# Optimization experiments

Hardware: AMD Instinct MI355X
Metric: run time of the kernel (lower is better)

## Reference

```python
import jax, jax.numpy as jnp
import numpy as np

N, E, B, L = 32768, 524288, 64, 4
ESM, S, V, EH = 1280, 128, 16, 64
N_RBF = 16
CENTERS = jnp.linspace(0.0, 12.0, N_RBF)
GAMMA = 1.0 / ((12.0 / N_RBF) ** 2 + 1e-8)
LN_EPS = 1e-5


def setup_inputs() -> dict:
    key = jax.random.key(0)
    ks = iter(jax.random.split(key, 80))
    def w(shape, scale=0.02):
        return (jax.random.normal(next(ks), shape) * scale).astype(jnp.float32)
    def zeros(shape):
        return jnp.zeros(shape, jnp.float32)
    def ones(shape):
        return jnp.ones(shape, jnp.float32)
    inp = {}
    inp['x_esm'] = jax.random.normal(next(ks), (N, ESM), jnp.float32)
    inp['x_reschem'] = jax.random.normal(next(ks), (N, 6), jnp.float32)
    inp['x_role'] = jax.random.uniform(next(ks), (N, 2), jnp.float32)
    inp['x_dist_raw'] = jax.random.uniform(next(ks), (N, 4), jnp.float32) * 12.0
    inp['x_misc'] = jax.random.normal(next(ks), (N, 3), jnp.float32)
    inp['x_vec'] = jax.random.normal(next(ks), (N, 1, 3), jnp.float32)
    inp['pos'] = jax.random.normal(next(ks), (N, 3), jnp.float32) * 10.0
    inp['edge_dist_raw'] = jax.random.uniform(next(ks), (E, 2), jnp.float32) * 12.0
    # node scalar encoder
    inp['ne_esm_w'] = w((ESM, 128)); inp['ne_esm_b'] = zeros((128,))
    inp['ne_esm_ln_g'] = ones((128,)); inp['ne_esm_ln_b'] = zeros((128,))
    in_dim = 128 + 6 + 2 + 3 + 4 * N_RBF  # 203
    inp['ne_out_w'] = w((in_dim, S)); inp['ne_out_b'] = zeros((S,))
    inp['ne_out_ln_g'] = ones((S,)); inp['ne_out_ln_b'] = zeros((S,))
    # edge scalar encoder
    inp['ee_w'] = w((2 * N_RBF, EH)); inp['ee_b'] = zeros((EH,))
    inp['ee_ln_g'] = ones((EH,)); inp['ee_ln_b'] = zeros((EH,))
    inp['init_vec_w'] = w((1, V))
    # stacked per-layer params
    msi = 2 * S + EH + 1 + (2 * V + 1)  # scalar_mlp in for message gvp = 354
    usi = 2 * S + 2 * V                 # = 288
    inp['msg_s_w1'] = w((L, msi, S)); inp['msg_s_b1'] = zeros((L, S))
    inp['msg_s_w2'] = w((L, S, S)); inp['msg_s_b2'] = zeros((L, S))
    inp['msg_v_w'] = w((L, 2 * V + 1, V))
    inp['msg_g_w'] = w((L, S, V)); inp['msg_g_b'] = zeros((L, V))
    inp['upd_s_w1'] = w((L, usi, S)); inp['upd_s_b1'] = zeros((L, S))
    inp['upd_s_w2'] = w((L, S, S)); inp['upd_s_b2'] = zeros((L, S))
    inp['upd_v_w'] = w((L, 2 * V, V))
    inp['upd_g_w'] = w((L, S, V)); inp['upd_g_b'] = zeros((L, V))
    inp['ln_g'] = ones((L, S)); inp['ln_b'] = zeros((L, S))
    # heads
    inp['hm_w1'] = w((2 * S, S)); inp['hm_b1'] = zeros((S,))
    inp['hm_w2'] = w((S, 8)); inp['hm_b2'] = zeros((8,))
    inp['he_w1'] = w((2 * S, S)); inp['he_b1'] = zeros((S,))
    inp['he_w2'] = w((S, 7)); inp['he_b2'] = zeros((7,))
    inp['edge_index'] = jax.random.randint(next(ks), (2, E), 0, N, jnp.int32)
    inp['batch'] = jnp.sort(jax.random.randint(next(ks), (N,), 0, B, jnp.int32))
    return inp


def _ln(x, g, b):
    mu = x.mean(-1, keepdims=True)
    var = ((x - mu) ** 2).mean(-1, keepdims=True)
    return (x - mu) * jax.lax.rsqrt(var + LN_EPS) * g + b


def _rbf(d):
    # d [..., K] -> [..., K, N_RBF]
    return jnp.exp(-GAMMA * (d[..., None] - CENTERS) ** 2)


def _vnorm(v):
    # v [N, C, 3] -> [N, C]
    return jnp.sqrt(jnp.clip((v * v).sum(-1), 1e-8))


def _gvp(s, v, sw1, sb1, sw2, sb2, vw, gw, gb):
    s_cat = jnp.concatenate([s, _vnorm(v)], -1)
    h = jax.nn.silu(s_cat @ sw1 + sb1)
    s_out = h @ sw2 + sb2
    v_proj = jnp.einsum('nci,cv->nvi', v, vw)
    gate = jax.nn.sigmoid(s_out @ gw + gb)[..., None]
    return s_out, v_proj * gate


def _forward(x_esm, x_reschem, x_role, x_dist_raw, x_misc, x_vec, pos, edge_dist_raw,
             ne_esm_w, ne_esm_b, ne_esm_ln_g, ne_esm_ln_b, ne_out_w, ne_out_b,
             ne_out_ln_g, ne_out_ln_b, ee_w, ee_b, ee_ln_g, ee_ln_b, init_vec_w,
             msg_s_w1, msg_s_b1, msg_s_w2, msg_s_b2, msg_v_w, msg_g_w, msg_g_b,
             upd_s_w1, upd_s_b1, upd_s_w2, upd_s_b2, upd_v_w, upd_g_w, upd_g_b,
             ln_g, ln_b, hm_w1, hm_b1, hm_w2, hm_b2, he_w1, he_b1, he_w2, he_b2,
             edge_index, batch):
    n = x_esm.shape[0]
    # node scalar encoder (dropout = identity at eval)
    esm = jax.nn.silu(_ln(x_esm @ ne_esm_w + ne_esm_b, ne_esm_ln_g, ne_esm_ln_b))
    d_rbf = _rbf(x_dist_raw).reshape(n, -1)  # [N, 64]
    xcat = jnp.concatenate([esm, x_reschem, x_role, x_misc, d_rbf], -1)
    s = jax.nn.silu(_ln(xcat @ ne_out_w + ne_out_b, ne_out_ln_g, ne_out_ln_b))
    # init vector channels [N, V, 3]
    v = jnp.einsum('nci,cv->nvi', x_vec, init_vec_w)
    # edge scalar encoder
    e_rbf = _rbf(edge_dist_raw).reshape(edge_dist_raw.shape[0], -1)  # [E, 32]
    edge_s = jax.nn.silu(_ln(e_rbf @ ee_w + ee_b, ee_ln_g, ee_ln_b))
    # edge vectors [E, 1, 3]
    src, dst = edge_index[0], edge_index[1]
    rel = pos[dst] - pos[src]
    rel = rel / jnp.sqrt(jnp.clip((rel * rel).sum(-1, keepdims=True), 1e-8))
    edge_v = rel[:, None, :]
    edge_len = _vnorm(edge_v)  # [E, 1]
    for l in range(L):
        m_s_in = jnp.concatenate([s[src], s[dst], edge_s, edge_len], -1)
        m_v_in = jnp.concatenate([v[src], v[dst], edge_v], 1)
        m_s, m_v = _gvp(m_s_in, m_v_in, msg_s_w1[l], msg_s_b1[l], msg_s_w2[l],
                        msg_s_b2[l], msg_v_w[l], msg_g_w[l], msg_g_b[l])
        agg_s = jax.ops.segment_sum(m_s, dst, num_segments=n)
        agg_v = jax.ops.segment_sum(m_v, dst, num_segments=n)
        u_s_in = jnp.concatenate([s, agg_s], -1)
        u_v_in = jnp.concatenate([v, agg_v], 1)
        ds, dv = _gvp(u_s_in, u_v_in, upd_s_w1[l], upd_s_b1[l], upd_s_w2[l],
                      upd_s_b2[l], upd_v_w[l], upd_g_w[l], upd_g_b[l])
        s = _ln(s + ds, ln_g[l], ln_b[l])
        v = v + dv
    # graph pooling
    sums = jax.ops.segment_sum(s, batch, num_segments=B)
    cnts = jax.ops.segment_sum(jnp.ones((n, 1), s.dtype), batch, num_segments=B)
    pooled_mean = sums / jnp.clip(cnts, 1.0)
    pooled_max = jax.ops.segment_max(s, batch, num_segments=B)
    pooled_max = jnp.where(jnp.isfinite(pooled_max), pooled_max, 0.0)
    embed = jnp.concatenate([pooled_mean, pooled_max], -1)
    logits_metal = jax.nn.silu(embed @ hm_w1 + hm_b1) @ hm_w2 + hm_b2
    logits_ec = jax.nn.silu(embed @ he_w1 + he_b1) @ he_w2 + he_b2
    return logits_metal, logits_ec, embed


def reference(x_esm, x_reschem, x_role, x_dist_raw, x_misc, x_vec, pos, edge_dist_raw,
              ne_esm_w, ne_esm_b, ne_esm_ln_g, ne_esm_ln_b, ne_out_w, ne_out_b,
              ne_out_ln_g, ne_out_ln_b, ee_w, ee_b, ee_ln_g, ee_ln_b, init_vec_w,
              msg_s_w1, msg_s_b1, msg_s_w2, msg_s_b2, msg_v_w, msg_g_w, msg_g_b,
              upd_s_w1, upd_s_b1, upd_s_w2, upd_s_b2, upd_v_w, upd_g_w, upd_g_b,
              ln_g, ln_b, hm_w1, hm_b1, hm_w2, hm_b2, he_w1, he_b1, he_w2, he_b2,
              edge_index, batch):
    return _forward(x_esm, x_reschem, x_role, x_dist_raw, x_misc, x_vec, pos,
                    edge_dist_raw, ne_esm_w, ne_esm_b, ne_esm_ln_g, ne_esm_ln_b,
                    ne_out_w, ne_out_b, ne_out_ln_g, ne_out_ln_b, ee_w, ee_b,
                    ee_ln_g, ee_ln_b, init_vec_w, msg_s_w1, msg_s_b1, msg_s_w2,
                    msg_s_b2, msg_v_w, msg_g_w, msg_g_b, upd_s_w1, upd_s_b1,
                    upd_s_w2, upd_s_b2, upd_v_w, upd_g_w, upd_g_b, ln_g, ln_b,
                    hm_w1, hm_b1, hm_w2, hm_b2, he_w1, he_b1, he_w2, he_b2,
                    edge_index, batch)
```

## Files before the change

### kernel.cpp

```cpp
#include <hip/hip_runtime.h>
#include <hip/hip_bf16.h>
#include <cstddef>

constexpr int kN = 32768;
constexpr int kE = 524288;
constexpr int kB = 64;
constexpr int kL = 4;
constexpr float kGamma = (float)(1.0 / (0.5625 + 1e-8));
constexpr float kLnEps = 1e-5f;

#define DI __device__ __forceinline__

typedef __attribute__((ext_vector_type(8))) short bf16x8;
typedef __attribute__((ext_vector_type(4))) short s16x4;
typedef __attribute__((ext_vector_type(4))) float f32x4;
#define MFMA16(a, b, c) __builtin_amdgcn_mfma_f32_16x16x32_bf16(a, b, c, 0, 0, 0)

DI float siluf(float x) { return x / (1.f + __expf(-x)); }
DI float sigmf(float x) { return 1.f / (1.f + __expf(-x)); }
DI unsigned short f2bf(float x) {
  __hip_bfloat16 b = __float2bfloat16(x);
  return *(unsigned short*)&b;
}
DI float b2f(unsigned short u) {
  union { unsigned i; float f; } c; c.i = ((unsigned)u) << 16; return c.f;
}
DI bf16x8 ldA(const float* p) {
  const float4 a = *(const float4*)p;
  const float4 b = *(const float4*)(p + 4);
  bf16x8 r;
  r[0] = (short)f2bf(a.x); r[1] = (short)f2bf(a.y);
  r[2] = (short)f2bf(a.z); r[3] = (short)f2bf(a.w);
  r[4] = (short)f2bf(b.x); r[5] = (short)f2bf(b.y);
  r[6] = (short)f2bf(b.z); r[7] = (short)f2bf(b.w);
  return r;
}

__global__ void k_btA(const float* src, unsigned short* dst, int K) {
  int idx = blockIdx.x * 256 + threadIdx.x;
  if (idx >= K * 128) return;
  int c = idx & 127, k = idx >> 7;
  dst[c * K + k] = f2bf(src[(size_t)k * 128 + c]);
}

__global__ void k_bt1(const float* w, unsigned short* dst) {
  int idx = blockIdx.x * 256 + threadIdx.x;
  int c = idx & 127, k = idx >> 7;
  dst[c * 224 + k] = f2bf(k < 203 ? w[(size_t)k * 128 + c] : 0.f);
}

__global__ void k_btPQ(const float* w1, unsigned short* dst) {
  int idx = blockIdx.x * 256 + threadIdx.x;
  int cc = idx / 160, k = idx - cc * 160;
  int c = cc & 127, half = cc >> 7;
  float v = 0.f;
  if (k < 128) v = w1[(size_t)(half * 128 + k) * 128 + c];
  else if (k < 144) v = w1[(size_t)(321 + half * 16 + (k - 128)) * 128 + c];
  dst[idx] = f2bf(v);
}

__global__ void k_w2gw(const float* w2, const float* gw, const float* b2, const float* gb,
                       float* out) {
  int idx = blockIdx.x * 256 + threadIdx.x;
  if (idx < 2048) {
    int k = idx >> 4, t = idx & 15;
    float a = 0.f;
    for (int j = 0; j < 128; j++) a += w2[(size_t)k * 128 + j] * gw[j * 16 + t];
    out[idx] = a;
  } else if (idx < 2064) {
    int t = idx - 2048;
    float a = gb[t];
    for (int j = 0; j < 128; j++) a += b2[j] * gw[j * 16 + t];
    out[idx] = a;
  }
}

__global__ void k_xrest(const float* resch, const float* role, const float* misc,
                        const float* dist, float* xr) {
  int idx = blockIdx.x * 256 + threadIdx.x;
  int r = idx / 96, c = idx - r * 96;
  float v = 0.f;
  if (c < 6) v = resch[r * 6 + c];
  else if (c < 8) v = role[r * 2 + c - 6];
  else if (c < 11) v = misc[r * 3 + c - 8];
  else if (c < 75) {
    int j = c - 11;
    float d = dist[r * 4 + (j >> 4)];
    float t = d - 0.8f * (float)(j & 15);
    v = __expf(-kGamma * t * t);
  }
  xr[idx] = v;
}

struct G2 {
  const float* A1; const float* A2; const float* A3;
  const unsigned short* BT;
  float* out;
  unsigned short* obfP; unsigned short* obfQ;
  const float* bias; const float* lng; const float* lnb;
};

template <int MODE>
__global__ __launch_bounds__(256) void k_gemm2(G2 p) {
  constexpr int K = MODE == 0 ? 1280 : MODE == 1 ? 224 : MODE == 2 ? 160 : 288;
  constexpr int NS = K / 32;
  constexpr int NTC = (MODE == 2) ? 16 : 8;
  const int tid = threadIdx.x, lane = tid & 63, wv = tid >> 6;
  const int g4 = lane >> 4, lc = lane & 15;
  const int r = blockIdx.x * 64 + wv * 16 + lc;
  const f32x4 z = {0.f, 0.f, 0.f, 0.f};
  f32x4 acc[NTC];
#pragma unroll
  for (int nt = 0; nt < NTC; nt++) acc[nt] = z;

  if constexpr (MODE == 0) {
#pragma unroll 4
    for (int ks = 0; ks < NS; ks++) {
      const int k = ks * 32 + g4 * 8;
      const bf16x8 af = ldA(p.A1 + (size_t)r * 1280 + k);
#pragma unroll
      for (int nt = 0; nt < NTC; nt++)
        acc[nt] = MFMA16(af, *(const bf16x8*)&p.BT[(lc + 16 * nt) * K + k], acc[nt]);
    }
  } else {
#pragma unroll
    for (int ks = 0; ks < NS; ks++) {
      const int k = ks * 32 + g4 * 8;
      const float* ap;
      if constexpr (MODE == 1)
        ap = (k < 128) ? p.A1 + (size_t)r * 128 + k : p.A2 + (size_t)r * 96 + (k - 128);
      else if constexpr (MODE == 2)
        ap = (k < 128) ? p.A1 + (size_t)r * 128 + k : p.A2 + (size_t)r * 32 + (k - 128);
      else
        ap = (k < 128) ? p.A1 + (size_t)r * 128 + k
           : (k < 256) ? p.A2 + (size_t)r * 128 + (k - 128)
                       : p.A3 + (size_t)r * 32 + (k - 256);
      const bf16x8 af = ldA(ap);
#pragma unroll
      for (int nt = 0; nt < NTC; nt++)
        acc[nt] = MFMA16(af, *(const bf16x8*)&p.BT[(lc + 16 * nt) * K + k], acc[nt]);
    }
  }

  const int row0 = blockIdx.x * 64 + wv * 16 + g4 * 4;
  if constexpr (MODE == 0 || MODE == 1) {
    float bias8[8], g8[8], b8[8];
#pragma unroll
    for (int nt = 0; nt < 8; nt++) {
      int c = lc + 16 * nt;
      bias8[nt] = p.bias[c]; g8[nt] = p.lng[c]; b8[nt] = p.lnb[c];
    }
    float rsum[4] = {0.f, 0.f, 0.f, 0.f}, rsq[4] = {0.f, 0.f, 0.f, 0.f};
#pragma unroll
    for (int nt = 0; nt < 8; nt++)
#pragma unroll
      for (int i = 0; i < 4; i++) {
        float x = acc[nt][i] + bias8[nt];
        acc[nt][i] = x; rsum[i] += x; rsq[i] += x * x;
      }
#pragma unroll
    for (int m = 1; m < 16; m <<= 1)
#pragma unroll
      for (int i = 0; i < 4; i++) {
        rsum[i] += __shfl_xor(rsum[i], m);
        rsq[i] += __shfl_xor(rsq[i], m);
      }
#pragma unroll
    for (int i = 0; i < 4; i++) {
      float mu = rsum[i] * (1.f / 128.f);
      float rs = rsqrtf(rsq[i] * (1.f / 128.f) - mu * mu + kLnEps);
#pragma unroll
      for (int nt = 0; nt < 8; nt++) {
        float y = (acc[nt][i] - mu) * rs * g8[nt] + b8[nt];
        p.out[(size_t)(row0 + i) * 128 + lc + 16 * nt] = siluf(y);
      }
    }
  } else if constexpr (MODE == 2) {
#pragma unroll
    for (int i = 0; i < 4; i++) {
      bf16x8 po, qo;
#pragma unroll
      for (int nt = 0; nt < 8; nt++) {
        po[nt] = (short)f2bf(acc[nt][i]);
        qo[nt] = (short)f2bf(acc[nt + 8][i] + p.bias[lc + 16 * nt]);
      }
      *(bf16x8*)&p.obfP[(size_t)(row0 + i) * 128 + lc * 8] = po;
      *(bf16x8*)&p.obfQ[(size_t)(row0 + i) * 128 + lc * 8] = qo;
    }
  } else {
#pragma unroll
    for (int nt = 0; nt < 8; nt++) {
      float bv = p.bias[lc + 16 * nt];
#pragma unroll
      for (int i = 0; i < 4; i++)
        p.out[(size_t)(row0 + i) * 128 + lc + 16 * nt] = siluf(acc[nt][i] + bv);
    }
  }
}

__global__ void k_v0(const float* xv, const float* ivw, float* v) {
  int idx = blockIdx.x * 256 + threadIdx.x;
  int n = idx / 48, f = idx % 48, t = f / 3, i = f - t * 3;
  v[idx] = xv[n * 3 + i] * ivw[t];
}

__global__ void k_vn(const float* v, float* vn) {
  int idx = blockIdx.x * 256 + threadIdx.x;
  int n = idx >> 5, t = idx & 31;
  float val = 0.f;
  if (t < 16) {
    const float* b = &v[(size_t)n * 48 + t * 3];
    val = sqrtf(fmaxf(b[0] * b[0] + b[1] * b[1] + b[2] * b[2], 1e-8f));
  }
  vn[idx] = val;
}

__global__ void k_vab(const float* v, const float* vw,
                      unsigned short* VAb, unsigned short* VBb) {
  int idx = blockIdx.x * 256 + threadIdx.x;
  int n = idx >> 4, t = idx & 15;
  float a0 = 0.f, a1 = 0.f, a2 = 0.f, b0 = 0.f, b1 = 0.f, b2 = 0.f;
#pragma unroll
  for (int c = 0; c < 16; c++) {
    float wa = vw[c * 16 + t], wb = vw[(16 + c) * 16 + t];
    float x0 = v[(size_t)n * 48 + c * 3 + 0];
    float x1 = v[(size_t)n * 48 + c * 3 + 1];
    float x2 = v[(size_t)n * 48 + c * 3 + 2];
    a0 += x0 * wa; a1 += x1 * wa; a2 += x2 * wa;
    b0 += x0 * wb; b1 += x1 * wb; b2 += x2 * wb;
  }
  s16x4 A, Bv;
  A[0] = (short)f2bf(a0); A[1] = (short)f2bf(a1); A[2] = (short)f2bf(a2); A[3] = 0;
  Bv[0] = (short)f2bf(b0); Bv[1] = (short)f2bf(b1); Bv[2] = (short)f2bf(b2); Bv[3] = 0;
  *(s16x4*)&VAb[(size_t)n * 64 + t * 4] = A;
  *(s16x4*)&VBb[(size_t)n * 64 + t * 4] = Bv;
}

__global__ void k_hist(const int* ei, int* cnt) {
  int e = blockIdx.x * 256 + threadIdx.x;
  atomicAdd(&cnt[ei[kE + e]], 1);
}

__global__ __launch_bounds__(1024) void k_scan(const int* cnt, int* rowstart, int* cursor) {
  __shared__ int part[1024];
  const int t = threadIdx.x;
  const int base = t * 32;
  int loc[32];
  int s = 0;
#pragma unroll
  for (int i = 0; i < 32; i++) { loc[i] = cnt[base + i]; s += loc[i]; }
  part[t] = s;
  __syncthreads();
  for (int off = 1; off < 1024; off <<= 1) {
    int val = (t >= off) ? part[t - off] : 0;
    __syncthreads();
    part[t] += val;
    __syncthreads();
  }
  int run = (t == 0) ? 0 : part[t - 1];
#pragma unroll
  for (int i = 0; i < 32; i++) {
    rowstart[base + i] = run;
    cursor[base + i] = run;
    run += loc[i];
  }
  if (t == 1023) rowstart[kN] = run;
}

__global__ void k_scatter(const int* ei, const float* pos, int* cursor,
                          int* prm, int* srcp, float* relp, float* lenp) {
  int e = blockIdx.x * 256 + threadIdx.x;
  int a = ei[e], b = ei[kE + e];
  int p = atomicAdd(&cursor[b], 1);
  prm[p] = e;
  srcp[p] = a;
  float dx = pos[(size_t)b * 3 + 0] - pos[(size_t)a * 3 + 0];
  float dy = pos[(size_t)b * 3 + 1] - pos[(size_t)a * 3 + 1];
  float dz = pos[(size_t)b * 3 + 2] - pos[(size_t)a * 3 + 2];
  float n2 = dx * dx + dy * dy + dz * dz;
  float inv = 1.f / sqrtf(fmaxf(n2, 1e-8f));
  float rx = dx * inv, ry = dy * inv, rz = dz * inv;
  relp[(size_t)p * 3 + 0] = rx; relp[(size_t)p * 3 + 1] = ry; relp[(size_t)p * 3 + 2] = rz;
  lenp[p] = sqrtf(fmaxf(rx * rx + ry * ry + rz * rz, 1e-8f));
}

__global__ void k_enc_perm(const int* prm, const float* edr, const float* eew, const float* eeb,
                           const float* lg, const float* lb, __hip_bfloat16* enc) {
  int tid = threadIdx.x;
  int wave = tid >> 6, lane = tid & 63;
  size_t p = (size_t)blockIdx.x * 4 + wave;
  int e = prm[p];
  __shared__ float rb[4][32];
  if (lane < 32) {
    float d = edr[(size_t)e * 2 + (lane >> 4)];
    float t = d - 0.8f * (float)(lane & 15);
    rb[wave][lane] = __expf(-kGamma * t * t);
  }
  __syncthreads();
  float acc = eeb[lane];
#pragma unroll 8
  for (int k = 0; k < 32; k++) acc += rb[wave][k] * eew[k * 64 + lane];
  float s = acc;
#pragma unroll
  for (int off = 32; off >= 1; off >>= 1) s += __shfl_xor(s, off);
  float mu = s * (1.f / 64.f);
  float d0 = acc - mu;
  float q = d0 * d0;
#pragma unroll
  for (int off = 32; off >= 1; off >>= 1) q += __shfl_xor(q, off);
  float rs = rsqrtf(q * (1.f / 64.f) + kLnEps);
  float y = d0 * rs * lg[lane] + lb[lane];
  enc[p * 64 + lane] = __float2bfloat16(siluf(y));
}

struct __align__(16) EMS2 {
  unsigned short we1T[128 * 72];
  unsigned short w2T[128 * 136];
  unsigned short w2gwT[16 * 72];
  unsigned short h[8][16 * 72];
  float wlen[128];
  float b2[128];
  float gb[16];
  float vw32[16];
};

__global__ __launch_bounds__(512, 4) void k_node_msg(
    const unsigned short* __restrict__ Pb, const unsigned short* __restrict__ Qb,
    const unsigned short* __restrict__ VAb, const unsigned short* __restrict__ VBb,
    const __hip_bfloat16* __restrict__ enc_, const float* __restrict__ relp,
    const float* __restrict__ lenp, const int* __restrict__ srcp,
    const int* __restrict__ rowstart, const float* __restrict__ vglob,
    const float* __restrict__ w1, const float* __restrict__ w2g,
    const float* __restrict__ b2g, const float* __restrict__ w2gw,
    const float* __restrict__ vwg,
    float* __restrict__ aggs, float* __restrict__ aggv, float* __restrict__ vnu) {
  __shared__ EMS2 sm;
  const int tid = threadIdx.x;
  const unsigned short* enc = (const unsigned short*)enc_;

#pragma unroll
  for (int i = 0; i < 16; i++) {
    int idx = tid + i * 512; int k = idx >> 7, n = idx & 127;
    sm.we1T[n * 72 + k] = f2bf(w1[(size_t)(256 + k) * 128 + n]);
  }
#pragma unroll
  for (int i = 0; i < 32; i++) {
    int idx = tid + i * 512; int k = idx >> 7, n = idx & 127;
    sm.w2T[n * 136 + k] = f2bf(w2g[(size_t)k * 128 + n]);
  }
#pragma unroll
  for (int i = 0; i < 4; i++) {
    int idx = tid + i * 512; int k = idx >> 4, t = idx & 15;
    sm.w2gwT[t * 72 + k] = f2bf(w2gw[k * 16 + t]);
  }
  if (tid < 128) { sm.wlen[tid] = w1[320 * 128 + tid] + w1[353 * 128 + tid]; sm.b2[tid] = b2g[tid]; }
  if (tid < 16) { sm.gb[tid] = w2gw[2048 + tid]; sm.vw32[tid] = vwg[512 + tid]; }
  __syncthreads();

  const int lane = tid & 63, wv = tid >> 6;
  const int g4 = lane >> 4;
  const int lc = lane & 15;
  unsigned short* hrow = &sm.h[wv][0];

  float wlenR[8], b2R[8];
#pragma unroll
  for (int nt = 0; nt < 8; nt++) { wlenR[nt] = sm.wlen[lc + 16 * nt]; b2R[nt] = sm.b2[lc + 16 * nt]; }
  const float gbR = sm.gb[lc];
  const float vwR = sm.vw32[lc];
  const f32x4 z = {0.f, 0.f, 0.f, 0.f};

  for (int n = blockIdx.x * 8 + wv; n < kN; n += gridDim.x * 8) {
    const int r0 = rowstart[n], r1 = rowstart[n + 1];
    float qR[8], vbR[3];
    {
      const bf16x8 qv = *(const bf16x8*)&Qb[(size_t)n * 128 + lc * 8];
#pragma unroll
      for (int nt = 0; nt < 8; nt++) qR[nt] = b2f((unsigned short)qv[nt]);
      const s16x4 vbv = *(const s16x4*)&VBb[(size_t)n * 64 + lc * 4];
#pragma unroll
      for (int j = 0; j < 3; j++) vbR[j] = b2f((unsigned short)vbv[j]);
    }
    float colsum[8];
#pragma unroll
    for (int nt = 0; nt < 8; nt++) colsum[nt] = 0.f;
    float av0 = 0.f, av1 = 0.f, av2 = 0.f;

    for (int base = r0; base < r1; base += 16) {
      int nv = r1 - base; if (nv > 16) nv = 16;

      int pa = base + lc; if (pa >= kE) pa = kE - 1;
      const bf16x8 a0 = *(const bf16x8*)&enc[(size_t)pa * 64 + g4 * 8];
      const bf16x8 a1 = *(const bf16x8*)&enc[(size_t)pa * 64 + 32 + g4 * 8];
      f32x4 acc[8];
#pragma unroll
      for (int nt = 0; nt < 8; nt++) {
        acc[nt] = MFMA16(a0, *(const bf16x8*)&sm.we1T[(lc + 16 * nt) * 72 + g4 * 8], z);
        acc[nt] = MFMA16(a1, *(const bf16x8*)&sm.we1T[(lc + 16 * nt) * 72 + 32 + g4 * 8], acc[nt]);
      }

      int sn[4], pr[4]; float le[4];
#pragma unroll
      for (int i = 0; i < 4; i++) {
        int p = base + g4 * 4 + i; if (p >= kE) p = kE - 1;
        pr[i] = p; sn[i] = srcp[p]; le[i] = lenp[p];
      }
#pragma unroll
      for (int i = 0; i < 4; i++) {
        const bf16x8 pbv = *(const bf16x8*)&Pb[(size_t)sn[i] * 128 + lc * 8];
#pragma unroll
        for (int nt = 0; nt < 8; nt++)
          acc[nt][i] += b2f((unsigned short)pbv[nt]) + qR[nt] + le[i] * wlenR[nt];
      }

      f32x4 m[8]; f32x4 gac;
#pragma unroll
      for (int i = 0; i < 4; i++)
#pragma unroll
        for (int nt = 0; nt < 4; nt++)
          hrow[(g4 * 4 + i) * 72 + lc + 16 * nt] = f2bf(siluf(acc[nt][i]));
      {
        const bf16x8 aB0 = *(const bf16x8*)&hrow[lc * 72 + g4 * 8];
        const bf16x8 aB1 = *(const bf16x8*)&hrow[lc * 72 + 32 + g4 * 8];
#pragma unroll
        for (int nt = 0; nt < 8; nt++) {
          m[nt] = MFMA16(aB0, *(const bf16x8*)&sm.w2T[(lc + 16 * nt) * 136 + g4 * 8], z);
          m[nt] = MFMA16(aB1, *(const bf16x8*)&sm.w2T[(lc + 16 * nt) * 136 + 32 + g4 * 8], m[nt]);
        }
        gac = MFMA16(aB0, *(const bf16x8*)&sm.w2gwT[lc * 72 + g4 * 8], z);
        gac = MFMA16(aB1, *(const bf16x8*)&sm.w2gwT[lc * 72 + 32 + g4 * 8], gac);
      }
#pragma unroll
      for (int i = 0; i < 4; i++)
#pragma unroll
        for (int nt = 4; nt < 8; nt++)
          hrow[(g4 * 4 + i) * 72 + lc + 16 * (nt - 4)] = f2bf(siluf(acc[nt][i]));
      {
        const bf16x8 aB2 = *(const bf16x8*)&hrow[lc * 72 + g4 * 8];
        const bf16x8 aB3 = *(const bf16x8*)&hrow[lc * 72 + 32 + g4 * 8];
#pragma unroll
        for (int nt = 0; nt < 8; nt++) {
          m[nt] = MFMA16(aB2, *(const bf16x8*)&sm.w2T[(lc + 16 * nt) * 136 + 64 + g4 * 8], m[nt]);
          m[nt] = MFMA16(aB3, *(const bf16x8*)&sm.w2T[(lc + 16 * nt) * 136 + 96 + g4 * 8], m[nt]);
        }
        gac = MFMA16(aB2, *(const bf16x8*)&sm.w2gwT[lc * 72 + 64 + g4 * 8], gac);
        gac = MFMA16(aB3, *(const bf16x8*)&sm.w2gwT[lc * 72 + 96 + g4 * 8], gac);
      }
#pragma unroll
      for (int nt = 0; nt < 8; nt++) {
#pragma unroll
        for (int i = 0; i < 4; i++) m[nt][i] += b2R[nt];
      }

#pragma unroll
      for (int i = 0; i < 4; i++) {
        const int row = g4 * 4 + i;
        if (row < nv) {
#pragma unroll
          for (int nt = 0; nt < 8; nt++) colsum[nt] += m[nt][i];
          float g = sigmf(gac[i] + gbR);
          const s16x4 vav = *(const s16x4*)&VAb[(size_t)sn[i] * 64 + lc * 4];
          const float* rp = &relp[(size_t)pr[i] * 3];
          av0 += g * (b2f((unsigned short)vav[0]) + vbR[0] + rp[0] * vwR);
          av1 += g * (b2f((unsigned short)vav[1]) + vbR[1] + rp[1] * vwR);
          av2 += g * (b2f((unsigned short)vav[2]) + vbR[2] + rp[2] * vwR);
        }
      }
    }

#pragma unroll
    for (int nt = 0; nt < 8; nt++) {
      colsum[nt] += __shfl_xor(colsum[nt], 16);
      colsum[nt] += __shfl_xor(colsum[nt], 32);
    }
    av0 += __shfl_xor(av0, 16); av0 += __shfl_xor(av0, 32);
    av1 += __shfl_xor(av1, 16); av1 += __shfl_xor(av1, 32);
    av2 += __shfl_xor(av2, 16); av2 += __shfl_xor(av2, 32);

    if (g4 == 0) {
#pragma unroll
      for (int nt = 0; nt < 8; nt++) aggs[(size_t)n * 128 + lc + 16 * nt] = colsum[nt];
      aggv[(size_t)n * 48 + lc * 3 + 0] = av0;
      aggv[(size_t)n * 48 + lc * 3 + 1] = av1;
      aggv[(size_t)n * 48 + lc * 3 + 2] = av2;
      vnu[(size_t)n * 32 + 16 + lc] = sqrtf(fmaxf(av0 * av0 + av1 * av1 + av2 * av2, 1e-8f));
    } else if (g4 == 1) {
      float x0 = vglob[(size_t)n * 48 + lc * 3 + 0];
      float x1 = vglob[(size_t)n * 48 + lc * 3 + 1];
      float x2 = vglob[(size_t)n * 48 + lc * 3 + 2];
      vnu[(size_t)n * 32 + lc] = sqrtf(fmaxf(x0 * x0 + x1 * x1 + x2 * x2, 1e-8f));
    }
  }
}

__global__ __launch_bounds__(256) void k_upd2(
    const float* __restrict__ hupd, const unsigned short* __restrict__ BuT,
    const float* __restrict__ b2,
    const float* __restrict__ ugw, const float* __restrict__ ugb, const float* __restrict__ uvw,
    const float* __restrict__ aggv, const float* __restrict__ lng, const float* __restrict__ lnb,
    float* __restrict__ s, float* __restrict__ v, float* __restrict__ vnout) {
  __shared__ __align__(16) float dsb[64 * 129];
  __shared__ float smu[64], srs[64];
  __shared__ float uvwS[512];
  const int tid = threadIdx.x;
  const int bm = blockIdx.x * 64;
  const int lane = tid & 63, wv = tid >> 6;
  const int g4 = lane >> 4, lc = lane & 15;
  uvwS[tid] = uvw[tid]; uvwS[tid + 256] = uvw[tid + 256];
  const f32x4 z = {0.f, 0.f, 0.f, 0.f};
  const int r = bm + wv * 16 + lc;
  f32x4 acc[8];
#pragma unroll
  for (int nt = 0; nt < 8; nt++) acc[nt] = z;

#pragma unroll
  for (int ks = 0; ks < 4; ks++) {
    const int k = ks * 32 + g4 * 8;
    const bf16x8 af = ldA(hupd + (size_t)r * 128 + k);
#pragma unroll
    for (int nt = 0; nt < 8; nt++)
      acc[nt] = MFMA16(af, *(const bf16x8*)&BuT[(lc + 16 * nt) * 128 + k], acc[nt]);
  }
#pragma unroll
  for (int nt = 0; nt < 8; nt++) {
    float bv = b2[lc + 16 * nt];
#pragma unroll
    for (int i = 0; i < 4; i++)
      dsb[(wv * 16 + g4 * 4 + i) * 129 + lc + 16 * nt] = acc[nt][i] + bv;
  }
  __syncthreads();

  const int rr = tid >> 2, p = tid & 3;
  const int n = bm + rr;
  float g[4];
#pragma unroll
  for (int j = 0; j < 4; j++) g[j] = ugb[p * 4 + j];
#pragma unroll 8
  for (int k = 0; k < 128; k++) {
    float m = dsb[rr * 129 + k];
    const float4 wg = *(const float4*)&ugw[k * 16 + p * 4];
    g[0] += m * wg.x; g[1] += m * wg.y; g[2] += m * wg.z; g[3] += m * wg.w;
  }
#pragma unroll
  for (int j = 0; j < 4; j++) g[j] = sigmf(g[j]);

  float vnew[12];
#pragma unroll
  for (int i2 = 0; i2 < 3; i2++) {
    float xv[16], xa[16];
#pragma unroll
    for (int c = 0; c < 16; c++) {
      xv[c] = v[(size_t)n * 48 + c * 3 + i2];
      xa[c] = aggv[(size_t)n * 48 + c * 3 + i2];
    }
#pragma unroll
    for (int j = 0; j < 4; j++) {
      int t = p * 4 + j;
      float a = 0.f;
#pragma unroll
      for (int c = 0; c < 16; c++)
        a += xv[c] * uvwS[c * 16 + t] + xa[c] * uvwS[(16 + c) * 16 + t];
      vnew[j * 3 + i2] = xv[t] + a * g[j];
    }
  }
  if (tid < 64) {
    float sm = 0.f, sq = 0.f;
    for (int c = 0; c < 128; c++) {
      float x = s[(size_t)(bm + tid) * 128 + c] + dsb[tid * 129 + c];
      sm += x; sq += x * x;
    }
    float mu = sm * (1.f / 128.f);
    float var = sq * (1.f / 128.f) - mu * mu;
    smu[tid] = mu; srs[tid] = rsqrtf(var + kLnEps);
  }
  __syncthreads();
#pragma unroll
  for (int j = 0; j < 4; j++) {
    float n0 = vnew[j * 3 + 0], n1 = vnew[j * 3 + 1], n2 = vnew[j * 3 + 2];
#pragma unroll
    for (int i2 = 0; i2 < 3; i2++)
      v[(size_t)n * 48 + (p * 4 + j) * 3 + i2] = vnew[j * 3 + i2];
    vnout[(size_t)n * 32 + p * 4 + j] = sqrtf(fmaxf(n0 * n0 + n1 * n1 + n2 * n2, 1e-8f));
    vnout[(size_t)n * 32 + 16 + p * 4 + j] = 0.f;
  }
#pragma unroll 4
  for (int i = 0; i < 32; i++) {
    int idx = tid + i * 256; int rw = idx >> 7, c = idx & 127;
    float x = s[(size_t)(bm + rw) * 128 + c] + dsb[rw * 129 + c];
    float y = (x - smu[rw]) * srs[rw] * lng[c] + lnb[c];
    s[(size_t)(bm + rw) * 128 + c] = y;
  }
}

DI int lbound(const int* b, int nn, int key) {
  int lo = 0, hi = nn;
  while (lo < hi) { int m = (lo + hi) >> 1; if (b[m] < key) lo = m + 1; else hi = m; }
  return lo;
}

__global__ void k_pool(const float* s, const int* batch, float* dout) {
  int g = blockIdx.x, tid = threadIdx.x;
  int lo = lbound(batch, kN, g), hi = lbound(batch, kN, g + 1);
  float sum = 0.f, mx = -3.402823e38f;
  for (int n = lo; n < hi; n++) {
    float x = s[(size_t)n * 128 + tid];
    sum += x; mx = fmaxf(mx, x);
  }
  int cnt = hi - lo;
  float mean = sum / fmaxf((float)cnt, 1.f);
  if (cnt == 0) mx = 0.f;
  dout[960 + g * 256 + tid] = mean;
  dout[960 + g * 256 + 128 + tid] = mx;
}

__global__ void k_heads(const float* hw1, const float* hb1, const float* hw2, const float* hb2,
                        const float* ew1, const float* eb1, const float* ew2, const float* eb2,
                        float* dout) {
  __shared__ float emb[256], h1[256];
  int g = blockIdx.x, tid = threadIdx.x;
  emb[tid] = dout[960 + g * 256 + tid];
  emb[128 + tid] = dout[960 + g * 256 + 128 + tid];
  __syncthreads();
  float am = hb1[tid], ae = eb1[tid];
#pragma unroll 4
  for (int k = 0; k < 256; k++) {
    float e = emb[k];
    am += e * hw1[k * 128 + tid];
    ae += e * ew1[k * 128 + tid];
  }
  h1[tid] = siluf(am); h1[128 + tid] = siluf(ae);
  __syncthreads();
  if (tid < 8) {
    float a = hb2[tid];
    for (int j = 0; j < 128; j++) a += h1[j] * hw2[j * 8 + tid];
    dout[g * 8 + tid] = a;
  } else if (tid >= 64 && tid < 71) {
    int o = tid - 64;
    float a = eb2[o];
    for (int j = 0; j < 128; j++) a += h1[128 + j] * ew2[j * 7 + o];
    dout[512 + g * 7 + o] = a;
  }
}

extern "C" void kernel_launch(void* const* d_in, const int* in_sizes, int n_in,
                              void* d_out, int out_size, void* d_ws, size_t ws_size,
                              hipStream_t stream) {
  (void)in_sizes; (void)n_in; (void)out_size; (void)ws_size;
  const float* x_esm   = (const float*)d_in[0];
  const float* x_resch = (const float*)d_in[1];
  const float* x_role  = (const float*)d_in[2];
  const float* x_dist  = (const float*)d_in[3];
  const float* x_misc  = (const float*)d_in[4];
  const float* x_vec   = (const float*)d_in[5];
  const float* pos     = (const float*)d_in[6];
  const float* edr     = (const float*)d_in[7];
  const float* ne_esm_w = (const float*)d_in[8];
  const float* ne_esm_b = (const float*)d_in[9];
  const float* ne_esm_lg = (const float*)d_in[10];
  const float* ne_esm_lb = (const float*)d_in[11];
  const float* ne_out_w = (const float*)d_in[12];
  const float* ne_out_b = (const float*)d_in[13];
  const float* ne_out_lg = (const float*)d_in[14];
  const float* ne_out_lb = (const float*)d_in[15];
  const float* ee_w = (const float*)d_in[16];
  const float* ee_b = (const float*)d_in[17];
  const float* ee_lg = (const float*)d_in[18];
  const float* ee_lb = (const float*)d_in[19];
  const float* ivw = (const float*)d_in[20];
  const float* msg_w1 = (const float*)d_in[21];
  const float* msg_b1 = (const float*)d_in[22];
  const float* msg_w2 = (const float*)d_in[23];
  const float* msg_b2 = (const float*)d_in[24];
  const float* msg_vw = (const float*)d_in[25];
  const float* msg_gw = (const float*)d_in[26];
  const float* msg_gb = (const float*)d_in[27];
  const float* upd_w1 = (const float*)d_in[28];
  const float* upd_b1 = (const float*)d_in[29];
  const float* upd_w2 = (const float*)d_in[30];
  const float* upd_b2 = (const float*)d_in[31];
  const float* upd_vw = (const float*)d_in[32];
  const float* upd_gw = (const float*)d_in[33];
  const float* upd_gb = (const float*)d_in[34];
  const float* ln_g = (const float*)d_in[35];
  const float* ln_b = (const float*)d_in[36];
  const float* hm_w1 = (const float*)d_in[37];
  const float* hm_b1 = (const float*)d_in[38];
  const float* hm_w2 = (const float*)d_in[39];
  const float* hm_b2 = (const float*)d_in[40];
  const float* he_w1 = (const float*)d_in[41];
  const float* he_b1 = (const float*)d_in[42];
  const float* he_w2 = (const float*)d_in[43];
  const float* he_b2 = (const float*)d_in[44];
  const int* ei = (const int*)d_in[45];
  const int* batch = (const int*)d_in[46];
  float* dout = (float*)d_out;

  size_t off = 0;
  auto alloc = [&](size_t bytes) {
    void* p = (char*)d_ws + off;
    off += (bytes + 255) & ~(size_t)255;
    return p;
  };
  float* s    = (float*)alloc((size_t)kN * 128 * 4);
  float* v    = (float*)alloc((size_t)kN * 48 * 4);
  float* vn   = (float*)alloc((size_t)kN * 32 * 4);
  unsigned short* Pb = (unsigned short*)alloc((size_t)kN * 128 * 2);
  unsigned short* Qb = (unsigned short*)alloc((size_t)kN * 128 * 2);
  unsigned short* VAb = (unsigned short*)alloc((size_t)kN * 64 * 2);
  unsigned short* VBb = (unsigned short*)alloc((size_t)kN * 64 * 2);
  float* aggS = (float*)alloc((size_t)kN * 128 * 4);
  float* aggV = (float*)alloc((size_t)kN * 48 * 4);
  float* vnu  = (float*)alloc((size_t)kN * 32 * 4);
  float* hupd = (float*)alloc((size_t)kN * 128 * 4);
  float* xrest = (float*)alloc((size_t)kN * 96 * 4);
  __hip_bfloat16* enc = (__hip_bfloat16*)alloc((size_t)kE * 64 * 2);
  float* relp = (float*)alloc((size_t)kE * 3 * 4);
  float* lenp = (float*)alloc((size_t)kE * 4);
  int* srcp   = (int*)alloc((size_t)kE * 4);
  int* prm    = (int*)alloc((size_t)kE * 4);
  int* cnt    = (int*)alloc((size_t)kN * 4);
  int* rowstart = (int*)alloc((size_t)(kN + 1) * 4);
  int* cursor = (int*)alloc((size_t)kN * 4);
  unsigned short* B0T = (unsigned short*)alloc((size_t)128 * 1280 * 2);
  unsigned short* B1T = (unsigned short*)alloc((size_t)128 * 224 * 2);
  unsigned short* B23T = (unsigned short*)alloc((size_t)kL * 256 * 160 * 2);
  unsigned short* B4T = (unsigned short*)alloc((size_t)kL * 128 * 288 * 2);
  unsigned short* BuT = (unsigned short*)alloc((size_t)kL * 128 * 128 * 2);
  float* w2gwL = (float*)alloc((size_t)kL * 2064 * 4);
  float* esm = hupd;

  hipMemsetAsync(cnt, 0, (size_t)kN * 4, stream);
  k_hist<<<kE / 256, 256, 0, stream>>>(ei, cnt);
  k_scan<<<1, 1024, 0, stream>>>(cnt, rowstart, cursor);
  k_scatter<<<kE / 256, 256, 0, stream>>>(ei, pos, cursor, prm, srcp, relp, lenp);
  k_enc_perm<<<kE / 4, 256, 0, stream>>>(prm, edr, ee_w, ee_b, ee_lg, ee_lb, enc);
  k_btA<<<(1280 * 128 + 255) / 256, 256, 0, stream>>>(ne_esm_w, B0T, 1280);
  k_bt1<<<(224 * 128 + 255) / 256, 256, 0, stream>>>(ne_out_w, B1T);
  k_xrest<<<(kN * 96 + 255) / 256, 256, 0, stream>>>(x_resch, x_role, x_misc, x_dist, xrest);
  for (int l = 0; l < kL; l++) {
    k_btPQ<<<(256 * 160 + 255) / 256, 256, 0, stream>>>(msg_w1 + (size_t)l * 354 * 128,
                                                        B23T + (size_t)l * 256 * 160);
    k_btA<<<(288 * 128 + 255) / 256, 256, 0, stream>>>(upd_w1 + (size_t)l * 288 * 128,
                                                       B4T + (size_t)l * 128 * 288, 288);
    k_btA<<<(128 * 128 + 255) / 256, 256, 0, stream>>>(upd_w2 + (size_t)l * 128 * 128,
                                                       BuT + (size_t)l * 128 * 128, 128);
    k_w2gw<<<9, 256, 0, stream>>>(msg_w2 + (size_t)l * 128 * 128, msg_gw + l * 128 * 16,
                                  msg_b2 + l * 128, msg_gb + l * 16, w2gwL + (size_t)l * 2064);
  }

  {
    G2 p{}; p.A1 = x_esm; p.BT = B0T; p.out = esm;
    p.bias = ne_esm_b; p.lng = ne_esm_lg; p.lnb = ne_esm_lb;
    k_gemm2<0><<<kN / 64, 256, 0, stream>>>(p);
  }
  {
    G2 p{}; p.A1 = esm; p.A2 = xrest; p.BT = B1T; p.out = s;
    p.bias = ne_out_b; p.lng = ne_out_lg; p.lnb = ne_out_lb;
    k_gemm2<1><<<kN / 64, 256, 0, stream>>>(p);
  }
  k_v0<<<kN * 48 / 256, 256, 0, stream>>>(x_vec, ivw, v);
  k_vn<<<kN * 32 / 256, 256, 0, stream>>>(v, vn);

  for (int l = 0; l < kL; l++) {
    const float* w1l = msg_w1 + (size_t)l * 354 * 128;
    const float* b1l = msg_b1 + l * 128;
    const float* w2l = msg_w2 + (size_t)l * 128 * 128;
    const float* b2l = msg_b2 + l * 128;
    const float* vwl = msg_vw + l * 33 * 16;
    const float* ub1 = upd_b1 + l * 128;
    const float* ub2 = upd_b2 + l * 128;
    const float* uvwl = upd_vw + l * 32 * 16;
    const float* ugwl = upd_gw + l * 128 * 16;
    const float* ugbl = upd_gb + l * 16;
    const float* lgl = ln_g + l * 128;
    const float* lbl = ln_b + l * 128;

    {
      G2 p{}; p.A1 = s; p.A2 = vn; p.BT = B23T + (size_t)l * 256 * 160;
      p.obfP = Pb; p.obfQ = Qb; p.bias = b1l;
      k_gemm2<2><<<kN / 64, 256, 0, stream>>>(p);
    }
    k_vab<<<kN * 16 / 256, 256, 0, stream>>>(v, vwl, VAb, VBb);
    k_node_msg<<<512, 512, 0, stream>>>(Pb, Qb, VAb, VBb, enc, relp, lenp, srcp,
                                        rowstart, v, w1l, w2l, b2l,
                                        w2gwL + (size_t)l * 2064, vwl,
                                        aggS, aggV, vnu);
    {
      G2 p{}; p.A1 = s; p.A2 = aggS; p.A3 = vnu; p.BT = B4T + (size_t)l * 128 * 288;
      p.out = hupd; p.bias = ub1;
      k_gemm2<4><<<kN / 64, 256, 0, stream>>>(p);
    }
    k_upd2<<<kN / 64, 256, 0, stream>>>(hupd, BuT + (size_t)l * 128 * 128, ub2,
                                        ugwl, ugbl, uvwl, aggV, lgl, lbl, s, v, vn);
  }

  k_pool<<<kB, 128, 0, stream>>>(s, batch, dout);
  k_heads<<<kB, 128, 0, stream>>>(hm_w1, hm_b1, hm_w2, hm_b2,
                                  he_w1, he_b1, he_w2, he_b2, dout);
}
```

Before: 1.889 ms.

## Compute edge RBF encoder with MFMA over 64 edges per block

The edge scalar encoder used one wave per edge with a scalar 32-term dot product and shuffle reductions, and one block per four edges. It now handles 64 edges per block and computes the RBF-by-weight product with bf16 16x16x32 MFMA, using a transposed weight tile held in shared memory. LayerNorm uses a single-pass sum and sum-of-squares reduction across 16 lanes. This cuts per-edge instruction count and block count, at the cost of bf16 rounding of the RBF features and weights and a less stable variance formula.

```diff
diff --git a/kernel.cpp b/kernel.cpp
--- a/kernel.cpp
+++ b/kernel.cpp
@@ -284,33 +284,72 @@
   lenp[p] = sqrtf(fmaxf(rx * rx + ry * ry + rz * rz, 1e-8f));
 }
 
-__global__ void k_enc_perm(const int* prm, const float* edr, const float* eew, const float* eeb,
-                           const float* lg, const float* lb, __hip_bfloat16* enc) {
-  int tid = threadIdx.x;
-  int wave = tid >> 6, lane = tid & 63;
-  size_t p = (size_t)blockIdx.x * 4 + wave;
-  int e = prm[p];
-  __shared__ float rb[4][32];
-  if (lane < 32) {
-    float d = edr[(size_t)e * 2 + (lane >> 4)];
-    float t = d - 0.8f * (float)(lane & 15);
-    rb[wave][lane] = __expf(-kGamma * t * t);
+__global__ __launch_bounds__(256) void k_enc_mfma(
+    const int* __restrict__ prm, const float* __restrict__ edr,
+    const float* __restrict__ eew, const float* __restrict__ eeb,
+    const float* __restrict__ lg, const float* __restrict__ lb,
+    __hip_bfloat16* __restrict__ enc) {
+  __shared__ unsigned short eewT[64 * 32];
+  const int tid = threadIdx.x;
+#pragma unroll
+  for (int i = 0; i < 8; i++) {
+    int idx = tid + i * 256;
+    int col = idx >> 5, k = idx & 31;
+    eewT[col * 32 + k] = f2bf(eew[k * 64 + col]);
   }
   __syncthreads();
-  float acc = eeb[lane];
-#pragma unroll 8
-  for (int k = 0; k < 32; k++) acc += rb[wave][k] * eew[k * 64 + lane];
-  float s = acc;
-#pragma unroll
-  for (int off = 32; off >= 1; off >>= 1) s += __shfl_xor(s, off);
-  float mu = s * (1.f / 64.f);
-  float d0 = acc - mu;
-  float q = d0 * d0;
-#pragma unroll
-  for (int off = 32; off >= 1; off >>= 1) q += __shfl_xor(q, off);
-  float rs = rsqrtf(q * (1.f / 64.f) + kLnEps);
-  float y = d0 * rs * lg[lane] + lb[lane];
-  enc[p * 64 + lane] = __float2bfloat16(siluf(y));
+
+  const int lane = tid & 63, wv = tid >> 6;
+  const int g4 = lane >> 4, lc = lane & 15;
+  const int e0 = blockIdx.x * 64 + wv * 16;
+
+  const int e = prm[e0 + lc];
+  const float d = edr[(size_t)e * 2 + (g4 >> 1)];
+  const float c0 = 0.8f * (float)((g4 & 1) * 8);
+  bf16x8 af;
+#pragma unroll
+  for (int j = 0; j < 8; j++) {
+    float t = d - (c0 + 0.8f * (float)j);
+    af[j] = (short)f2bf(__expf(-kGamma * t * t));
+  }
+  const f32x4 z = {0.f, 0.f, 0.f, 0.f};
+  f32x4 acc[4];
+#pragma unroll
+  for (int ct = 0; ct < 4; ct++)
+    acc[ct] = MFMA16(af, *(const bf16x8*)&eewT[(ct * 16 + lc) * 32 + g4 * 8], z);
+
+  float bias4[4], g4v[4], b4[4];
+#pragma unroll
+  for (int ct = 0; ct < 4; ct++) {
+    int col = ct * 16 + lc;
+    bias4[ct] = eeb[col]; g4v[ct] = lg[col]; b4[ct] = lb[col];
+  }
+  float rsum[4] = {0.f, 0.f, 0.f, 0.f}, rsq[4] = {0.f, 0.f, 0.f, 0.f};
+#pragma unroll
+  for (int ct = 0; ct < 4; ct++)
+#pragma unroll
+    for (int i = 0; i < 4; i++) {
+      float x = acc[ct][i] + bias4[ct];
+      acc[ct][i] = x; rsum[i] += x; rsq[i] += x * x;
+    }
+#pragma unroll
+  for (int m = 1; m < 16; m <<= 1)
+#pragma unroll
+    for (int i = 0; i < 4; i++) {
+      rsum[i] += __shfl_xor(rsum[i], m);
+      rsq[i] += __shfl_xor(rsq[i], m);
+    }
+#pragma unroll
+  for (int i = 0; i < 4; i++) {
+    float mu = rsum[i] * (1.f / 64.f);
+    float rs = rsqrtf(rsq[i] * (1.f / 64.f) - mu * mu + kLnEps);
+    const size_t row = (size_t)(e0 + g4 * 4 + i);
+#pragma unroll
+    for (int ct = 0; ct < 4; ct++) {
+      float y = (acc[ct][i] - mu) * rs * g4v[ct] + b4[ct];
+      enc[row * 64 + ct * 16 + lc] = __float2bfloat16(siluf(y));
+    }
+  }
 }
 
 struct __align__(16) EMS2 {
@@ -732,7 +771,7 @@
   k_hist<<<kE / 256, 256, 0, stream>>>(ei, cnt);
   k_scan<<<1, 1024, 0, stream>>>(cnt, rowstart, cursor);
   k_scatter<<<kE / 256, 256, 0, stream>>>(ei, pos, cursor, prm, srcp, relp, lenp);
-  k_enc_perm<<<kE / 4, 256, 0, stream>>>(prm, edr, ee_w, ee_b, ee_lg, ee_lb, enc);
+  k_enc_mfma<<<kE / 64, 256, 0, stream>>>(prm, edr, ee_w, ee_b, ee_lg, ee_lb, enc);
   k_btA<<<(1280 * 128 + 255) / 256, 256, 0, stream>>>(ne_esm_w, B0T, 1280);
   k_bt1<<<(224 * 128 + 255) / 256, 256, 0, stream>>>(ne_out_w, B1T);
   k_xrest<<<(kN * 96 + 255) / 256, 256, 0, stream>>>(x_resch, x_role, x_misc, x_dist, xrest);
```

After: 1.747 ms. 1.08x faster.
